# Kernel tuning notes

Hardware: AMD Instinct MI355X
Metric: run time of the kernel (lower is better)

## Reference

```python
import jax, jax.numpy as jnp
import numpy as np

H = 1024  # hidden_size
B, S = 64, 2048


def setup_inputs() -> dict:
    key = jax.random.key(0)
    ks = jax.random.split(key, 9)
    d = {
        "s_t": jax.random.normal(ks[0], (B, 2 * H), jnp.float32),
        "h_i": jax.random.normal(ks[1], (B, S, 2 * H), jnp.float32),
        "coverage": jax.random.uniform(ks[2], (B, S), jnp.float32),
        # parameters (torch Linear: y = x @ W.T + b)
        "W_h": jax.random.normal(ks[3], (H, 2 * H), jnp.float32) / np.sqrt(2 * H),
        "b_h": jnp.zeros((H,), jnp.float32),
        "W_s": jax.random.normal(ks[4], (H, 2 * H), jnp.float32) / np.sqrt(2 * H),
        "b_s": jnp.zeros((H,), jnp.float32),
        "W_c": jax.random.normal(ks[5], (H, 1), jnp.float32),  # no bias
        "v_a": jax.random.normal(ks[6], (1, H), jnp.float32) / np.sqrt(H),
        "b_a": jnp.zeros((1,), jnp.float32),
    }
    return d


def reference(s_t, h_i, coverage, W_h, b_h, W_s, b_s, W_c, v_a, b_a):
    # Wi_hi: (B,S,H)
    Wi_hi = jnp.einsum("bsd,hd->bsh", h_i, W_h) + b_h
    # Ws_s: (B,H)
    Ws_s = jnp.einsum("bd,hd->bh", s_t, W_s) + b_s
    # coverage features: (B,S,H)  (W_c is (H,1))
    cov_feat = coverage[:, :, None] * W_c[:, 0]
    # scores: (B,S)
    E = jnp.einsum("bsh,h->bs", jnp.tanh(Wi_hi + Ws_s[:, None, :] + cov_feat), v_a[0]) + b_a[0]
    A = jax.nn.softmax(E, axis=-1)
    # context: (B,2H)
    C = jnp.einsum("bs,bsd->bd", A, h_i)
    new_cov = coverage + A
    return (C, A, new_cov)
```

## Files before the change

kernel.cpp:

```cpp
#include <hip/hip_runtime.h>
#include <hip/hip_bf16.h>

typedef __bf16 bf16x8_v __attribute__((ext_vector_type(8)));
typedef float  f32x4_v  __attribute__((ext_vector_type(4)));

static constexpr int kH = 1024;
static constexpr int kD = 2048;
static constexpr int kB = 64;
static constexpr int kS = 2048;
static constexpr int kM = kB * kS;

__device__ __forceinline__ void load_lds16(const void* g, void* l) {
  __builtin_amdgcn_global_load_lds(
      (const __attribute__((address_space(1))) unsigned int*)g,
      (__attribute__((address_space(3))) unsigned int*)l, 16, 0, 0);
}

__device__ __forceinline__ float fast_tanh(float x) {
  float e = __expf(2.0f * x);
  return 1.0f - 2.0f * __builtin_amdgcn_rcpf(e + 1.0f);
}

__global__ __launch_bounds__(256) void conv_tile_kernel(const float* __restrict__ in,
                                                        __bf16* __restrict__ out) {
  size_t g = (size_t)blockIdx.x * 256 + threadIdx.x;
  int p = (int)(g & 63);
  size_t tile = g >> 6;
  int kt = (int)(tile & 63);
  size_t mt16 = tile >> 6;
  int rr = p >> 2, s = p & 3;
  int c = s ^ ((rr >> 1) & 3);
  const float* src = in + (mt16 * 16 + rr) * (size_t)kD + kt * 32 + c * 8;
  float4 v0 = reinterpret_cast<const float4*>(src)[0];
  float4 v1 = reinterpret_cast<const float4*>(src)[1];
  bf16x8_v o = {(__bf16)v0.x, (__bf16)v0.y, (__bf16)v0.z, (__bf16)v0.w,
                (__bf16)v1.x, (__bf16)v1.y, (__bf16)v1.z, (__bf16)v1.w};
  reinterpret_cast<bf16x8_v*>(out)[g] = o;
}

__global__ __launch_bounds__(256) void prep_bias_kernel(
    const float* __restrict__ s_t, const float* __restrict__ W_s,
    const float* __restrict__ b_s, const float* __restrict__ b_h,
    float* __restrict__ biasBH) {
  int wave = blockIdx.x * 4 + (threadIdx.x >> 6);
  int lane = threadIdx.x & 63;
  int b = wave >> 10, h = wave & 1023;
  const float4* sp = reinterpret_cast<const float4*>(s_t + (size_t)b * kD);
  const float4* wp = reinterpret_cast<const float4*>(W_s + (size_t)h * kD);
  float acc = 0.f;
  for (int i = lane; i < kD / 4; i += 64) {
    float4 a = sp[i], w = wp[i];
    acc += a.x * w.x + a.y * w.y + a.z * w.z + a.w * w.w;
  }
  for (int m = 1; m < 64; m <<= 1) acc += __shfl_xor(acc, m);
  if (lane == 0) biasBH[wave] = acc + b_s[h] + b_h[h];
}

__global__ __launch_bounds__(512, 2) void gemm_score_kernel(
    const float* __restrict__ h_i,
    const __bf16* __restrict__ Wtl,
    const float* __restrict__ biasBH,
    const float* __restrict__ coverage,
    const float* __restrict__ Wc,
    const float* __restrict__ va,
    float* __restrict__ E) {
  const int bid = blockIdx.x;
  const int xcd = bid & 7;
  const int slot = bid >> 3;
  const int nblk = slot & 3;
  const int n0 = nblk * 256;
  const int m0 = (xcd * 64 + (slot >> 2)) * 256;

  const int tid = threadIdx.x;
  const int lane = tid & 63;
  const int wid = tid >> 6;
  const int wm = wid >> 2, wn = wid & 3;

  __shared__ __align__(16) char lds[81920];

  f32x4_v acc[8][4];
#pragma unroll
  for (int m = 0; m < 8; ++m)
#pragma unroll
    for (int n = 0; n < 4; ++n) acc[m][n] = {0.f, 0.f, 0.f, 0.f};

  const int l15 = lane & 15;
  const int j = lane >> 4;
  const int slot16 = (j ^ ((l15 >> 1) & 3)) << 4;

  const int arow = wid * 32 + (lane >> 1);
  const int ah = lane & 1;
  const float* Ag = h_i + (size_t)(m0 + arow) * kD + ah * 16;
  const int ast = arow >> 4;
  const int arr = arow & 15;
  const int ax = (arr >> 1) & 3;
  const int aw0 = ast * 1024 + arr * 64 + (((2 * ah) ^ ax) << 4);
  const int aw1 = ast * 1024 + arr * 64 + (((2 * ah + 1) ^ ax) << 4);

  const __bf16* Bsrc0 = Wtl + ((size_t)(nblk * 16 + wid * 2) * 64) * 512 + lane * 8;
  const __bf16* Bsrc1 = Wtl + ((size_t)(nblk * 16 + wid * 2 + 1) * 64) * 512 + lane * 8;

  f32x4_v avP[4], avQ[4];

#define LOADA(T, AV)                                                  \
  do {                                                                \
    const float* p_ = Ag + (size_t)(T) * 32;                          \
    AV[0] = *reinterpret_cast<const f32x4_v*>(p_);                    \
    AV[1] = *reinterpret_cast<const f32x4_v*>(p_ + 4);                \
    AV[2] = *reinterpret_cast<const f32x4_v*>(p_ + 8);                \
    AV[3] = *reinterpret_cast<const f32x4_v*>(p_ + 12);               \
  } while (0)

#define WRITEA(AV, BUF)                                               \
  do {                                                                \
    char* base_ = lds + (BUF) * 16384;                                \
    bf16x8_v o0_ = {(__bf16)AV[0][0], (__bf16)AV[0][1], (__bf16)AV[0][2], (__bf16)AV[0][3], \
                    (__bf16)AV[1][0], (__bf16)AV[1][1], (__bf16)AV[1][2], (__bf16)AV[1][3]}; \
    bf16x8_v o1_ = {(__bf16)AV[2][0], (__bf16)AV[2][1], (__bf16)AV[2][2], (__bf16)AV[2][3], \
                    (__bf16)AV[3][0], (__bf16)AV[3][1], (__bf16)AV[3][2], (__bf16)AV[3][3]}; \
    *reinterpret_cast<bf16x8_v*>(base_ + aw0) = o0_;                  \
    *reinterpret_cast<bf16x8_v*>(base_ + aw1) = o1_;                  \
  } while (0)

#define GLOADB(T)                                                     \
  do {                                                                \
    char* bd_ = lds + 32768 + ((T) % 3) * 16384;                      \
    load_lds16(Bsrc0 + (size_t)(T) * 512, bd_ + (wid * 2) * 1024);    \
    load_lds16(Bsrc1 + (size_t)(T) * 512, bd_ + (wid * 2 + 1) * 1024);\
  } while (0)

#define TILE13(T, AVC, AVN)                                           \
  do {                                                                \
    asm volatile("s_waitcnt vmcnt(6)" ::: "memory");                  \
    asm volatile("s_waitcnt lgkmcnt(0)" ::: "memory");                \
    __builtin_amdgcn_s_barrier();                                     \
    __builtin_amdgcn_sched_barrier(0);                                \
    if ((T) + 2 < 64) {                                               \
      GLOADB((T) + 2);                                                \
      LOADA((T) + 2, AVN);                                            \
    }                                                                 \
    const char* Ab_ = lds + ((T) & 1) * 16384;                        \
    const char* Bb_ = lds + 32768 + ((T) % 3) * 16384;                \
    bf16x8_v b_[4], a_[4];                                            \
    _Pragma("unroll")                                                 \
    for (int n = 0; n < 4; ++n)                                       \
      b_[n] = *reinterpret_cast<const bf16x8_v*>(                     \
          Bb_ + (wn * 4 + n) * 1024 + l15 * 64 + slot16);             \
    _Pragma("unroll")                                                 \
    for (int mi = 0; mi < 4; ++mi)                                    \
      a_[mi] = *reinterpret_cast<const bf16x8_v*>(                    \
          Ab_ + (wm * 8 + mi) * 1024 + l15 * 64 + slot16);            \
    __builtin_amdgcn_s_setprio(1);                                    \
    _Pragma("unroll")                                                 \
    for (int mi = 0; mi < 4; ++mi)                                    \
      _Pragma("unroll")                                               \
      for (int n = 0; n < 4; ++n)                                     \
        acc[mi][n] = __builtin_amdgcn_mfma_f32_16x16x32_bf16(a_[mi], b_[n], acc[mi][n], 0, 0, 0); \
    __builtin_amdgcn_s_setprio(0);                                    \
    _Pragma("unroll")                                                 \
    for (int mi = 0; mi < 4; ++mi)                                    \
      a_[mi] = *reinterpret_cast<const bf16x8_v*>(                    \
          Ab_ + (wm * 8 + 4 + mi) * 1024 + l15 * 64 + slot16);        \
    __builtin_amdgcn_s_setprio(1);                                    \
    _Pragma("unroll")                                                 \
    for (int mi = 0; mi < 4; ++mi)                                    \
      _Pragma("unroll")                                               \
      for (int n = 0; n < 4; ++n)                                     \
        acc[4 + mi][n] = __builtin_amdgcn_mfma_f32_16x16x32_bf16(a_[mi], b_[n], acc[4 + mi][n], 0, 0, 0); \
    __builtin_amdgcn_s_setprio(0);                                    \
    if ((T) + 1 < 64) WRITEA(AVC, ((T) + 1) & 1);                     \
  } while (0)

  GLOADB(0);
  GLOADB(1);
  LOADA(0, avP);
  asm volatile("s_waitcnt vmcnt(0)" ::: "memory");
  WRITEA(avP, 0);
  LOADA(1, avP);

  for (int t = 0; t < 64; t += 2) {
    TILE13(t, avP, avQ);
    TILE13(t + 1, avQ, avP);
  }

#undef LOADA
#undef WRITEA
#undef GLOADB
#undef TILE13

  const int bb = m0 >> 11;
  const int colg = lane & 15;
  const int rowg = lane >> 4;
  float bias_v[4], wc_v[4], va_v[4];
#pragma unroll
  for (int n = 0; n < 4; ++n) {
    int h = n0 + wn * 64 + n * 16 + colg;
    bias_v[n] = biasBH[bb * kH + h];
    wc_v[n] = Wc[h];
    va_v[n] = va[h];
  }
  const int s_tile = (m0 & (kS - 1));
#pragma unroll
  for (int m = 0; m < 8; ++m) {
    int sbase = s_tile + wm * 128 + m * 16 + rowg * 4;
    float cov[4], rowsum[4];
#pragma unroll
    for (int q = 0; q < 4; ++q) {
      cov[q] = coverage[bb * kS + sbase + q];
      rowsum[q] = 0.f;
    }
#pragma unroll
    for (int n = 0; n < 4; ++n) {
#pragma unroll
      for (int q = 0; q < 4; ++q) {
        float z = acc[m][n][q] + bias_v[n] + cov[q] * wc_v[n];
        rowsum[q] += fast_tanh(z) * va_v[n];
      }
    }
#pragma unroll
    for (int q = 0; q < 4; ++q) {
      float v = rowsum[q];
      v += __shfl_xor(v, 1);
      v += __shfl_xor(v, 2);
      v += __shfl_xor(v, 4);
      v += __shfl_xor(v, 8);
      if (colg == 0) atomicAdd(&E[bb * kS + sbase + q], v);
    }
  }
}

__global__ __launch_bounds__(256) void softmax_kernel(
    const float* __restrict__ E, const float* __restrict__ coverage,
    float* __restrict__ A, float* __restrict__ newcov) {
  int b = blockIdx.x;
  int tid = threadIdx.x;
  int wid = tid >> 6, lane = tid & 63;
  __shared__ float wred[4];
  float ev[8];
  float mx = -INFINITY;
#pragma unroll
  for (int i = 0; i < 8; ++i) {
    ev[i] = E[b * kS + tid + i * 256];
    mx = fmaxf(mx, ev[i]);
  }
  for (int m = 1; m < 64; m <<= 1) mx = fmaxf(mx, __shfl_xor(mx, m));
  if (lane == 0) wred[wid] = mx;
  __syncthreads();
  mx = fmaxf(fmaxf(wred[0], wred[1]), fmaxf(wred[2], wred[3]));
  __syncthreads();
  float sum = 0.f;
#pragma unroll
  for (int i = 0; i < 8; ++i) {
    ev[i] = __expf(ev[i] - mx);
    sum += ev[i];
  }
  for (int m = 1; m < 64; m <<= 1) sum += __shfl_xor(sum, m);
  if (lane == 0) wred[wid] = sum;
  __syncthreads();
  sum = wred[0] + wred[1] + wred[2] + wred[3];
  float inv = 1.f / sum;
#pragma unroll
  for (int i = 0; i < 8; ++i) {
    int s = tid + i * 256;
    float a = ev[i] * inv;
    A[b * kS + s] = a;
    newcov[b * kS + s] = coverage[b * kS + s] + a;
  }
}

__global__ __launch_bounds__(256) void context_kernel(
    const float* __restrict__ h_i, const float* __restrict__ A,
    float* __restrict__ C) {
  int b = blockIdx.x;
  int d = blockIdx.y * 1024 + threadIdx.x * 4;
  int s0 = blockIdx.z * 256;
  const float* hp = h_i + ((size_t)b * kS + s0) * kD + d;
  const float* ap = A + b * kS + s0;
  float4 acc = {0.f, 0.f, 0.f, 0.f};
  for (int s = 0; s < 256; ++s) {
    float a = ap[s];
    float4 v = *reinterpret_cast<const float4*>(hp + (size_t)s * kD);
    acc.x += a * v.x;
    acc.y += a * v.y;
    acc.z += a * v.z;
    acc.w += a * v.w;
  }
  atomicAdd(&C[b * kD + d + 0], acc.x);
  atomicAdd(&C[b * kD + d + 1], acc.y);
  atomicAdd(&C[b * kD + d + 2], acc.z);
  atomicAdd(&C[b * kD + d + 3], acc.w);
}

extern "C" void kernel_launch(void* const* d_in, const int* in_sizes, int n_in,
                              void* d_out, int out_size, void* d_ws, size_t ws_size,
                              hipStream_t stream) {
  const float* s_t      = (const float*)d_in[0];
  const float* h_i      = (const float*)d_in[1];
  const float* coverage = (const float*)d_in[2];
  const float* W_h      = (const float*)d_in[3];
  const float* b_h      = (const float*)d_in[4];
  const float* W_s      = (const float*)d_in[5];
  const float* b_s      = (const float*)d_in[6];
  const float* W_c      = (const float*)d_in[7];
  const float* v_a      = (const float*)d_in[8];

  float* out = (float*)d_out;
  float* C      = out;
  float* A      = out + kB * kD;
  float* newcov = A + kB * kS;

  char* ws = (char*)d_ws;
  __bf16* Wtl   = (__bf16*)ws;
  float* biasBH = (float*)(ws + (4u << 20));
  float* E      = (float*)(ws + (4u << 20) + (256u << 10));

  hipMemsetAsync(E, 0, (size_t)kB * kS * sizeof(float), stream);
  hipMemsetAsync(C, 0, (size_t)kB * kD * sizeof(float), stream);

  conv_tile_kernel<<<kH, 256, 0, stream>>>(W_h, Wtl);
  prep_bias_kernel<<<(kB * kH) / 4, 256, 0, stream>>>(s_t, W_s, b_s, b_h, biasBH);

  gemm_score_kernel<<<2048, 512, 0, stream>>>(h_i, Wtl, biasBH, coverage,
                                              W_c, v_a, E);

  softmax_kernel<<<kB, 256, 0, stream>>>(E, coverage, A, newcov);

  dim3 gc(kB, kD / 1024, kS / 256);
  context_kernel<<<gc, 256, 0, stream>>>(h_i, A, C);
}
```

Baseline: 916.5 us.

## Shrink GEMM tile to 256x128 to double occupancy, single A register buffer

Halves the N-tile of the fused score GEMM from 256 to 128 columns. This halves accumulators per wave, shrinks the B staging buffers, and drops the double A register buffer in favour of writing A to LDS at the start of each step. Launch bounds move to 4 blocks per CU and the grid doubles, aiming to hide latency through occupancy. The cost is that the fp32 h_i reads and bf16 conversion are repeated across twice as many N-blocks, and there is less MFMA work per barrier.

```diff
diff --git a/kernel.cpp b/kernel.cpp
--- a/kernel.cpp
+++ b/kernel.cpp
@@ -56,7 +56,7 @@
   if (lane == 0) biasBH[wave] = acc + b_s[h] + b_h[h];
 }
 
-__global__ __launch_bounds__(512, 2) void gemm_score_kernel(
+__global__ __launch_bounds__(512, 4) void gemm_score_kernel(
     const float* __restrict__ h_i,
     const __bf16* __restrict__ Wtl,
     const float* __restrict__ biasBH,
@@ -67,20 +67,20 @@
   const int bid = blockIdx.x;
   const int xcd = bid & 7;
   const int slot = bid >> 3;
-  const int nblk = slot & 3;
-  const int n0 = nblk * 256;
-  const int m0 = (xcd * 64 + (slot >> 2)) * 256;
+  const int nblk = slot & 7;
+  const int n0 = nblk * 128;
+  const int m0 = (xcd * 64 + (slot >> 3)) * 256;
 
   const int tid = threadIdx.x;
   const int lane = tid & 63;
   const int wid = tid >> 6;
-  const int wm = wid >> 2, wn = wid & 3;
-
-  __shared__ __align__(16) char lds[81920];
-
-  f32x4_v acc[8][4];
-#pragma unroll
-  for (int m = 0; m < 8; ++m)
+  const int wm = wid >> 1, wn = wid & 1;
+
+  __shared__ __align__(16) char lds[57344];
+
+  f32x4_v acc[4][4];
+#pragma unroll
+  for (int m = 0; m < 4; ++m)
 #pragma unroll
     for (int n = 0; n < 4; ++n) acc[m][n] = {0.f, 0.f, 0.f, 0.f};
 
@@ -97,50 +97,45 @@
   const int aw0 = ast * 1024 + arr * 64 + (((2 * ah) ^ ax) << 4);
   const int aw1 = ast * 1024 + arr * 64 + (((2 * ah + 1) ^ ax) << 4);
 
-  const __bf16* Bsrc0 = Wtl + ((size_t)(nblk * 16 + wid * 2) * 64) * 512 + lane * 8;
-  const __bf16* Bsrc1 = Wtl + ((size_t)(nblk * 16 + wid * 2 + 1) * 64) * 512 + lane * 8;
-
-  f32x4_v avP[4], avQ[4];
-
-#define LOADA(T, AV)                                                  \
+  const __bf16* Bsrc = Wtl + ((size_t)(nblk * 8 + wid) * 64) * 512 + lane * 8;
+
+  f32x4_v av[4];
+
+#define LOADA(T)                                                      \
   do {                                                                \
     const float* p_ = Ag + (size_t)(T) * 32;                          \
-    AV[0] = *reinterpret_cast<const f32x4_v*>(p_);                    \
-    AV[1] = *reinterpret_cast<const f32x4_v*>(p_ + 4);                \
-    AV[2] = *reinterpret_cast<const f32x4_v*>(p_ + 8);                \
-    AV[3] = *reinterpret_cast<const f32x4_v*>(p_ + 12);               \
+    av[0] = *reinterpret_cast<const f32x4_v*>(p_);                    \
+    av[1] = *reinterpret_cast<const f32x4_v*>(p_ + 4);                \
+    av[2] = *reinterpret_cast<const f32x4_v*>(p_ + 8);                \
+    av[3] = *reinterpret_cast<const f32x4_v*>(p_ + 12);               \
   } while (0)
 
-#define WRITEA(AV, BUF)                                               \
+#define WRITEA(BUF)                                                   \
   do {                                                                \
     char* base_ = lds + (BUF) * 16384;                                \
-    bf16x8_v o0_ = {(__bf16)AV[0][0], (__bf16)AV[0][1], (__bf16)AV[0][2], (__bf16)AV[0][3], \
-                    (__bf16)AV[1][0], (__bf16)AV[1][1], (__bf16)AV[1][2], (__bf16)AV[1][3]}; \
-    bf16x8_v o1_ = {(__bf16)AV[2][0], (__bf16)AV[2][1], (__bf16)AV[2][2], (__bf16)AV[2][3], \
-                    (__bf16)AV[3][0], (__bf16)AV[3][1], (__bf16)AV[3][2], (__bf16)AV[3][3]}; \
+    bf16x8_v o0_ = {(__bf16)av[0][0], (__bf16)av[0][1], (__bf16)av[0][2], (__bf16)av[0][3], \
+                    (__bf16)av[1][0], (__bf16)av[1][1], (__bf16)av[1][2], (__bf16)av[1][3]}; \
+    bf16x8_v o1_ = {(__bf16)av[2][0], (__bf16)av[2][1], (__bf16)av[2][2], (__bf16)av[2][3], \
+                    (__bf16)av[3][0], (__bf16)av[3][1], (__bf16)av[3][2], (__bf16)av[3][3]}; \
     *reinterpret_cast<bf16x8_v*>(base_ + aw0) = o0_;                  \
     *reinterpret_cast<bf16x8_v*>(base_ + aw1) = o1_;                  \
   } while (0)
 
 #define GLOADB(T)                                                     \
+  load_lds16(Bsrc + (size_t)(T) * 512, lds + 32768 + ((T) % 3) * 8192 + wid * 1024)
+
+#define TILE14(T)                                                     \
   do {                                                                \
-    char* bd_ = lds + 32768 + ((T) % 3) * 16384;                      \
-    load_lds16(Bsrc0 + (size_t)(T) * 512, bd_ + (wid * 2) * 1024);    \
-    load_lds16(Bsrc1 + (size_t)(T) * 512, bd_ + (wid * 2 + 1) * 1024);\
-  } while (0)
-
-#define TILE13(T, AVC, AVN)                                           \
-  do {                                                                \
-    asm volatile("s_waitcnt vmcnt(6)" ::: "memory");                  \
     asm volatile("s_waitcnt lgkmcnt(0)" ::: "memory");                \
     __builtin_amdgcn_s_barrier();                                     \
     __builtin_amdgcn_sched_barrier(0);                                \
+    if ((T) + 1 < 64) WRITEA(((T) + 1) & 1);                          \
     if ((T) + 2 < 64) {                                               \
       GLOADB((T) + 2);                                                \
-      LOADA((T) + 2, AVN);                                            \
+      LOADA((T) + 2);                                                 \
     }                                                                 \
     const char* Ab_ = lds + ((T) & 1) * 16384;                        \
-    const char* Bb_ = lds + 32768 + ((T) % 3) * 16384;                \
+    const char* Bb_ = lds + 32768 + ((T) % 3) * 8192;                 \
     bf16x8_v b_[4], a_[4];                                            \
     _Pragma("unroll")                                                 \
     for (int n = 0; n < 4; ++n)                                       \
@@ -149,7 +144,7 @@
     _Pragma("unroll")                                                 \
     for (int mi = 0; mi < 4; ++mi)                                    \
       a_[mi] = *reinterpret_cast<const bf16x8_v*>(                    \
-          Ab_ + (wm * 8 + mi) * 1024 + l15 * 64 + slot16);            \
+          Ab_ + (wm * 4 + mi) * 1024 + l15 * 64 + slot16);            \
     __builtin_amdgcn_s_setprio(1);                                    \
     _Pragma("unroll")                                                 \
     for (int mi = 0; mi < 4; ++mi)                                    \
@@ -157,36 +152,24 @@
       for (int n = 0; n < 4; ++n)                                     \
         acc[mi][n] = __builtin_amdgcn_mfma_f32_16x16x32_bf16(a_[mi], b_[n], acc[mi][n], 0, 0, 0); \
     __builtin_amdgcn_s_setprio(0);                                    \
-    _Pragma("unroll")                                                 \
-    for (int mi = 0; mi < 4; ++mi)                                    \
-      a_[mi] = *reinterpret_cast<const bf16x8_v*>(                    \
-          Ab_ + (wm * 8 + 4 + mi) * 1024 + l15 * 64 + slot16);        \
-    __builtin_amdgcn_s_setprio(1);                                    \
-    _Pragma("unroll")                                                 \
-    for (int mi = 0; mi < 4; ++mi)                                    \
-      _Pragma("unroll")                                               \
-      for (int n = 0; n < 4; ++n)                                     \
-        acc[4 + mi][n] = __builtin_amdgcn_mfma_f32_16x16x32_bf16(a_[mi], b_[n], acc[4 + mi][n], 0, 0, 0); \
-    __builtin_amdgcn_s_setprio(0);                                    \
-    if ((T) + 1 < 64) WRITEA(AVC, ((T) + 1) & 1);                     \
   } while (0)
 
   GLOADB(0);
   GLOADB(1);
-  LOADA(0, avP);
+  LOADA(0);
   asm volatile("s_waitcnt vmcnt(0)" ::: "memory");
-  WRITEA(avP, 0);
-  LOADA(1, avP);
+  WRITEA(0);
+  LOADA(1);
 
   for (int t = 0; t < 64; t += 2) {
-    TILE13(t, avP, avQ);
-    TILE13(t + 1, avQ, avP);
+    TILE14(t);
+    TILE14(t + 1);
   }
 
 #undef LOADA
 #undef WRITEA
 #undef GLOADB
-#undef TILE13
+#undef TILE14
 
   const int bb = m0 >> 11;
   const int colg = lane & 15;
@@ -201,8 +184,8 @@
   }
   const int s_tile = (m0 & (kS - 1));
 #pragma unroll
-  for (int m = 0; m < 8; ++m) {
-    int sbase = s_tile + wm * 128 + m * 16 + rowg * 4;
+  for (int m = 0; m < 4; ++m) {
+    int sbase = s_tile + wm * 64 + m * 16 + rowg * 4;
     float cov[4], rowsum[4];
 #pragma unroll
     for (int q = 0; q < 4; ++q) {
@@ -320,7 +303,7 @@
   conv_tile_kernel<<<kH, 256, 0, stream>>>(W_h, Wtl);
   prep_bias_kernel<<<(kB * kH) / 4, 256, 0, stream>>>(s_t, W_s, b_s, b_h, biasBH);
 
-  gemm_score_kernel<<<2048, 512, 0, stream>>>(h_i, Wtl, biasBH, coverage,
+  gemm_score_kernel<<<4096, 512, 0, stream>>>(h_i, Wtl, biasBH, coverage,
                                               W_c, v_a, E);
 
   softmax_kernel<<<kB, 256, 0, stream>>>(E, coverage, A, newcov);
```

Result: slower. 979.5 us (+6.9%).
